# Performance work log

Hardware: AMD Instinct MI355X
Metric: run time of the kernel (lower is better)

Reference implementation:

```python
import jax, jax.numpy as jnp
import numpy as np

H = 2048        # hidden_dim
D = 128         # head_dim
NQ = H // D     # 16 query heads
NKV = 4         # kv heads (GQA)
ROTARY_BASE = 10000.0


def _rope_cos_sin(seq_len, dim, dtype):
    inv_freq = 1.0 / (ROTARY_BASE ** (jnp.arange(0, dim, 2, dtype=jnp.float32) / dim))
    t = jnp.arange(seq_len, dtype=jnp.float32)
    freqs = jnp.outer(t, inv_freq)          # [S, D/2]
    return jnp.cos(freqs).astype(dtype), jnp.sin(freqs).astype(dtype)


def _apply_rope(x, cos, sin):
    # x: [B, S, H, D], non-interleaved (rotate-half) convention of flash-attn
    d2 = x.shape[-1] // 2
    x1, x2 = x[..., :d2], x[..., d2:]
    c = cos[None, :, None, :]
    s = sin[None, :, None, :]
    return jnp.concatenate([x1 * c - x2 * s, x2 * c + x1 * s], axis=-1)


def setup_inputs() -> dict:
    key = jax.random.key(0)
    ks = jax.random.split(key, 9)
    B, S = 2, 2048
    sd = 1.0 / np.sqrt(H)
    return {
        "hidden_states": jax.random.normal(ks[0], (B, S, H), jnp.float32),
        "Wq": jax.random.normal(ks[1], (H, NQ * D), jnp.float32) * sd,
        "bq": jnp.zeros((NQ * D,), jnp.float32),
        "Wk": jax.random.normal(ks[2], (H, NKV * D), jnp.float32) * sd,
        "bk": jnp.zeros((NKV * D,), jnp.float32),
        "Wv": jax.random.normal(ks[3], (H, NKV * D), jnp.float32) * sd,
        "bv": jnp.zeros((NKV * D,), jnp.float32),
        "Wc": jax.random.normal(ks[4], (NQ * D, H), jnp.float32) * sd,
        "bc": jnp.zeros((H,), jnp.float32),
    }


def reference(hidden_states, Wq, bq, Wk, bk, Wv, bv, Wc, bc):
    B, S, _ = hidden_states.shape
    scale = 1.0 / np.sqrt(D)  # scale_attn_by_inverse_layer_idx=False

    q = (hidden_states @ Wq + bq).reshape(B, S, NQ, D)
    k = (hidden_states @ Wk + bk).reshape(B, S, NKV, D)
    v = (hidden_states @ Wv + bv).reshape(B, S, NKV, D)

    cos, sin = _rope_cos_sin(S, D, q.dtype)
    q = _apply_rope(q, cos, sin)
    k = _apply_rope(k, cos, sin)

    # GQA: expand kv heads to match query heads
    rep = NQ // NKV
    k_e = jnp.repeat(k, rep, axis=2)  # [B, S, NQ, D]
    v_e = jnp.repeat(v, rep, axis=2)

    scores = jnp.einsum("bshd,bthd->bhst", q, k_e) * scale  # [B, NQ, S, S]
    causal = jnp.tril(jnp.ones((S, S), bool))
    scores = jnp.where(causal[None, None], scores, jnp.finfo(scores.dtype).min)
    probs = jax.nn.softmax(scores, axis=-1)
    attn = jnp.einsum("bhst,bthd->bshd", probs, v_e)  # [B, S, NQ, D]

    out = attn.reshape(B, S, NQ * D) @ Wc + bc  # resid dropout p=0 (eval)
    return out, k, v
```

## Files before the change

### kernel.cpp

```cpp
#include <hip/hip_runtime.h>
#include <math.h>

typedef unsigned short u16;
typedef __attribute__((ext_vector_type(8))) short s16x8;
typedef __attribute__((ext_vector_type(4))) float f32x4;
typedef __attribute__((ext_vector_type(16))) float f32x16;

#define B_  2
#define S_  2048
#define H_  2048
#define D_  128
#define NQ_ 16
#define NKV_ 4
#define M_  (B_*S_)
#define NQKV_ 3072

#define MFMA16(a,b,c) __builtin_amdgcn_mfma_f32_16x16x32_bf16(a,b,c,0,0,0)
#define MFMA32(a,b,c) __builtin_amdgcn_mfma_f32_32x32x16_bf16(a,b,c,0,0,0)

__device__ __forceinline__ u16 f2bf(float x) {
  union { float f; unsigned u; } v; v.f = x;
  unsigned r = v.u + 0x7fffu + ((v.u >> 16) & 1u);
  return (u16)(r >> 16);
}
__device__ __forceinline__ float bf2f(u16 x) {
  union { unsigned u; float f; } v; v.u = ((unsigned)x) << 16;
  return v.f;
}

__device__ __forceinline__ unsigned cvtpk(float lo, float hi) {
  unsigned r;
  asm("v_cvt_pk_bf16_f32 %0, %1, %2" : "=v"(r) : "v"(lo), "v"(hi));
  return r;
}

__global__ __launch_bounds__(256) void cvt_x(const float* __restrict__ X, u16* __restrict__ Xb, long n4) {
  const f32x4* X4 = (const f32x4*)X;
  for (long i = (long)blockIdx.x*256 + threadIdx.x; i < n4; i += (long)gridDim.x*256) {
    f32x4 v = X4[i];
    union { u16 u[4]; unsigned long long ll; } p;
    p.u[0] = f2bf(v[0]); p.u[1] = f2bf(v[1]); p.u[2] = f2bf(v[2]); p.u[3] = f2bf(v[3]);
    ((unsigned long long*)Xb)[i] = p.ll;
  }
}

__global__ __launch_bounds__(256) void wtrans(const float* __restrict__ W, u16* __restrict__ Wt,
                                              int N, int K) {
  __shared__ float t[32][33];
  const int n0 = blockIdx.x*32, k0 = blockIdx.y*32;
  const int tx = threadIdx.x, ty = threadIdx.y;
  #pragma unroll
  for (int i = 0; i < 32; i += 8) t[ty+i][tx] = W[(long)(k0+ty+i)*N + n0 + tx];
  __syncthreads();
  #pragma unroll
  for (int i = 0; i < 32; i += 8) Wt[(long)(n0+ty+i)*K + k0 + tx] = f2bf(t[tx][ty+i]);
}

__global__ __launch_bounds__(256) void vtrans(const u16* __restrict__ QKV, u16* __restrict__ Vt) {
  __shared__ u16 t[32][33];
  const int bk = blockIdx.z;
  const int s0 = blockIdx.x*32, d0 = blockIdx.y*32;
  const int tx = threadIdx.x, ty = threadIdx.y;
  const int b = bk >> 2, kvh = bk & 3;
  #pragma unroll
  for (int i = 0; i < 32; i += 8)
    t[ty+i][tx] = QKV[(long)(b*S_ + s0+ty+i)*NQKV_ + 2560 + kvh*128 + d0 + tx];
  __syncthreads();
  #pragma unroll
  for (int i = 0; i < 32; i += 8)
    Vt[((long)bk*D_ + d0+ty+i)*S_ + s0 + tx] = t[tx][ty+i];
}

__global__ void concat_bias(const float* bq, const float* bk, const float* bv, float* bqkv) {
  int i = blockIdx.x*256 + threadIdx.x;
  if (i < NQKV_)
    bqkv[i] = (i < 2048) ? bq[i] : ((i < 2560) ? bk[i-2048] : bv[i-2560]);
}

__global__ void rope_tab(float* __restrict__ cosb, float* __restrict__ sinb) {
  int i = blockIdx.x*256 + threadIdx.x;
  int t = i >> 6, d = i & 63;
  float inv = powf(10000.0f, -((float)(2*d)) * (1.0f/128.0f));
  float fr = (float)t * inv;
  float sv, cv;
  sincosf(fr, &sv, &cv);
  cosb[i] = cv; sinb[i] = sv;
}

__global__ __launch_bounds__(256) void rope_qkv(
    const u16* __restrict__ QKV, const float* __restrict__ cosb, const float* __restrict__ sinb,
    u16* __restrict__ Qb, u16* __restrict__ Kb,
    float* __restrict__ kout, float* __restrict__ vout)
{
  const float QS = 0.08838834764831845f * 1.4426950408889634f;
  const int m = blockIdx.x;
  const int b = m >> 11, s = m & 2047;
  const int tid = threadIdx.x;
  const u16* row = QKV + (long)m * NQKV_;
  const int d = tid & 63;
  const float c  = cosb[s*64 + d];
  const float sn = sinb[s*64 + d];
  #pragma unroll
  for (int i = 0; i < 4; i++) {
    int hh = (tid + i*256) >> 6;
    float x1 = bf2f(row[hh*128 + d]), x2 = bf2f(row[hh*128 + d + 64]);
    float o1 = x1*c - x2*sn, o2 = x2*c + x1*sn;
    long base = ((long)(b*NQ_ + hh)*S_ + s)*D_;
    Qb[base + d] = f2bf(o1*QS);
    Qb[base + d + 64] = f2bf(o2*QS);
  }
  {
    int kh = tid >> 6;
    float x1 = bf2f(row[2048 + kh*128 + d]), x2 = bf2f(row[2048 + kh*128 + d + 64]);
    float o1 = x1*c - x2*sn, o2 = x2*c + x1*sn;
    long kb = ((long)(b*NKV_ + kh)*S_ + s)*D_;
    Kb[kb + d] = f2bf(o1);
    Kb[kb + d + 64] = f2bf(o2);
    long ko = ((long)m*NKV_ + kh)*D_;
    kout[ko + d] = o1;
    kout[ko + d + 64] = o2;
  }
  #pragma unroll
  for (int i = 0; i < 2; i++) {
    int e = tid + i*256;
    vout[(long)m*512 + e] = bf2f(row[2560 + e]);
  }
}

template<int BN, typename OutT>
__global__ __launch_bounds__(512, 2) void gemm256(
    const u16* __restrict__ A, const u16* __restrict__ Bm,
    const float* __restrict__ bias, OutT* __restrict__ C,
    int M, int N, int K)
{
  __shared__ u16 As[2][256*64];
  __shared__ u16 Bs[2][BN*64];
  constexpr int WCc = (BN == 256) ? 4 : 2;
  constexpr int MI  = (BN == 256) ? 8 : 4;
  constexpr int LB  = BN/64;
  constexpr int TOT = 4 + LB;

  const int tid = threadIdx.x;
  const int lane = tid & 63, w = tid >> 6;
  const int r16 = lane & 15, g = lane >> 4;
  const int wrn = w / WCc, wcn = w % WCc;
  const int abase = wrn * (MI*16);
  const int bbase = wcn * 64;

  const int gx = gridDim.x;
  const int nwg = gx * gridDim.y;
  const int id = blockIdx.y * gx + blockIdx.x;
  const int cpx = nwg >> 3;
  const int sid = (id & 7) * cpx + (id >> 3);
  const long m0 = (long)(sid / gx) * 256;
  const long n0 = (long)(sid % gx) * BN;

  const u16* Ag = A + m0 * K;
  const u16* Bg = Bm + n0 * K;

  auto stage = [&](int buf, int k0) {
    #pragma unroll
    for (int i = 0; i < 4; i++) {
      const int slot = i*512 + tid;
      const int row = slot >> 3, cg = slot & 7;
      const u16* src = Ag + (long)row*K + k0 + ((cg ^ (row & 7)) * 8);
      __builtin_amdgcn_global_load_lds(
          (const __attribute__((address_space(1))) unsigned int*)src,
          (__attribute__((address_space(3))) unsigned int*)&As[buf][slot*8], 16, 0, 0);
    }
    #pragma unroll
    for (int i = 0; i < LB; i++) {
      const int slot = i*512 + tid;
      const int row = slot >> 3, cg = slot & 7;
      const u16* src = Bg + (long)row*K + k0 + ((cg ^ (row & 7)) * 8);
      __builtin_amdgcn_global_load_lds(
          (const __attribute__((address_space(1))) unsigned int*)src,
          (__attribute__((address_space(3))) unsigned int*)&Bs[buf][slot*8], 16, 0, 0);
    }
  };

  f32x4 acc[MI][4] = {};
  const int nt = K >> 6;

  stage(0, 0);
  stage(1, 64);
  for (int t = 0; t < nt; t++) {
    if (t + 1 < nt) {
      if constexpr (TOT == 8) asm volatile("s_waitcnt vmcnt(8)" ::: "memory");
      else                    asm volatile("s_waitcnt vmcnt(6)" ::: "memory");
    } else {
      asm volatile("s_waitcnt vmcnt(0)" ::: "memory");
    }
    __builtin_amdgcn_s_barrier();

    const u16* as = &As[t & 1][0];
    const u16* bs = &Bs[t & 1][0];
    #pragma unroll
    for (int k = 0; k < 2; k++) {
      s16x8 bfr[4];
      #pragma unroll
      for (int nj = 0; nj < 4; nj++) {
        const int R = bbase + nj*16 + r16;
        bfr[nj] = *(const s16x8*)&bs[R*64 + (((k*4 + g) ^ (R & 7)) * 8)];
      }
      __builtin_amdgcn_s_setprio(1);
      #pragma unroll
      for (int mi = 0; mi < MI; mi++) {
        const int R = abase + mi*16 + r16;
        s16x8 afr = *(const s16x8*)&as[R*64 + (((k*4 + g) ^ (R & 7)) * 8)];
        #pragma unroll
        for (int nj = 0; nj < 4; nj++)
          acc[mi][nj] = MFMA16(afr, bfr[nj], acc[mi][nj]);
      }
      __builtin_amdgcn_s_setprio(0);
    }
    __builtin_amdgcn_s_barrier();
    if (t + 2 < nt) stage(t & 1, (t + 2) << 6);
  }

  #pragma unroll
  for (int mi = 0; mi < MI; mi++) {
    #pragma unroll
    for (int nj = 0; nj < 4; nj++) {
      const int col = bbase + nj*16 + r16;
      const float bv = bias[n0 + col];
      #pragma unroll
      for (int r = 0; r < 4; r++) {
        const long row = m0 + abase + mi*16 + g*4 + r;
        if constexpr (sizeof(OutT) == 2)
          C[row * N + n0 + col] = (OutT)f2bf(acc[mi][nj][r] + bv);
        else
          C[row * N + n0 + col] = (OutT)(acc[mi][nj][r] + bv);
      }
    }
  }
}

__global__ __launch_bounds__(256, 2) void attn_kernel(
    const u16* __restrict__ Qb, const u16* __restrict__ Kb,
    const u16* __restrict__ Vt, u16* __restrict__ Ob)
{
  __shared__ u16 Ks[2][64*128];
  __shared__ u16 Vs[2][128*64];
  const int tid = threadIdx.x;
  const int lane = tid & 63, w = tid >> 6;
  const int l31 = lane & 31, hi = lane >> 5;
  const int id = blockIdx.x;
  const int bh = id & 31;
  const int b = bh >> 4, h = bh & 15;
  const int p = id >> 5;
  const int qt = (p < 8) ? p : (23 - p);
  const int kvh = h >> 2;
  const int q0w = qt*128 + w*32;
  const int nt = 2*qt + 2;

  const u16* Qg = Qb + (((long)(b*NQ_ + h))*S_ + q0w)*D_;
  const u16* Kg = Kb + ((long)(b*NKV_ + kvh))*S_*D_;
  const u16* Vg = Vt + ((long)(b*NKV_ + kvh))*D_*S_;

  s16x8 qf[8];
  #pragma unroll
  for (int ks = 0; ks < 8; ks++)
    qf[ks] = *(const s16x8*)&Qg[l31*D_ + ks*16 + hi*8];

  f32x16 po[4] = {};
  float mrow = -1e30f, lrow = 0.f;

  auto stage = [&](int buf, int kv0s) {
    #pragma unroll
    for (int i = 0; i < 4; i++) {
      const int c = i*4 + w;
      const int G = c*64 + lane;
      const int krow = G >> 4, kcg = G & 15;
      const u16* gk = Kg + (long)(kv0s + krow)*D_ + ((kcg ^ (krow & 15)) * 8);
      __builtin_amdgcn_global_load_lds(
          (const __attribute__((address_space(1))) unsigned int*)gk,
          (__attribute__((address_space(3))) unsigned int*)&Ks[buf][c*512], 16, 0, 0);
      const int vrow = G >> 3, vcg = G & 7;
      const u16* gv = Vg + (long)vrow*S_ + kv0s + ((vcg ^ (vrow & 7)) * 8);
      __builtin_amdgcn_global_load_lds(
          (const __attribute__((address_space(1))) unsigned int*)gv,
          (__attribute__((address_space(3))) unsigned int*)&Vs[buf][c*512], 16, 0, 0);
    }
  };

  stage(0, 0);
  for (int t = 0; t < nt; t++) {
    const int cur = t & 1;
    const int kv0 = t*64;
    if (t + 1 < nt) {
      stage(cur ^ 1, kv0 + 64);
      asm volatile("s_waitcnt vmcnt(8)" ::: "memory");
    } else {
      asm volatile("s_waitcnt vmcnt(0)" ::: "memory");
    }
    __builtin_amdgcn_s_barrier();

    if (kv0 <= q0w + 31) {
      f32x16 sc[2] = {};
      #pragma unroll
      for (int ks = 0; ks < 8; ks++) {
        #pragma unroll
        for (int ct = 0; ct < 2; ct++) {
          const int row = ct*32 + l31;
          s16x8 kf = *(const s16x8*)&Ks[cur][row*128 + ((ks*16 + hi*8) ^ ((row & 15)*8))];
          sc[ct] = MFMA32(kf, qf[ks], sc[ct]);
        }
      }
      if (kv0 + 63 > q0w) {
        const int qrow = q0w + l31;
        #pragma unroll
        for (int ct = 0; ct < 2; ct++)
          #pragma unroll
          for (int r = 0; r < 16; r++) {
            int kv = kv0 + ct*32 + (r & 3) + 8*(r >> 2) + 4*hi;
            if (kv > qrow) sc[ct][r] = -3.0e38f;
          }
      }
      float pm = sc[0][0];
      #pragma unroll
      for (int ct = 0; ct < 2; ct++)
        #pragma unroll
        for (int r = 0; r < 16; r++) pm = fmaxf(pm, sc[ct][r]);
      pm = fmaxf(pm, __shfl_xor(pm, 32, 64));
      if (!__all(pm - mrow <= 8.0f)) {
        float mn = fmaxf(mrow, pm);
        float fr = exp2f(mrow - mn);
        mrow = mn;
        lrow *= fr;
        #pragma unroll
        for (int r = 0; r < 16; r++) {
          float frv = __shfl(fr, (r & 3) + 8*(r >> 2) + 4*hi, 64);
          #pragma unroll
          for (int dt = 0; dt < 4; dt++) po[dt][r] *= frv;
        }
      }
      float ps = 0.f;
      #pragma unroll
      for (int ct = 0; ct < 2; ct++)
        #pragma unroll
        for (int r = 0; r < 16; r++) {
          float pv = exp2f(sc[ct][r] - mrow);
          sc[ct][r] = pv;
          ps += pv;
        }
      ps += __shfl_xor(ps, 32, 64);
      lrow += ps;
      unsigned mw[2][8], ex[2][8];
      #pragma unroll
      for (int ct = 0; ct < 2; ct++)
        #pragma unroll
        for (int wd = 0; wd < 8; wd++)
          mw[ct][wd] = cvtpk(sc[ct][2*wd], sc[ct][2*wd + 1]);
      #pragma unroll
      for (int ct = 0; ct < 2; ct++)
        #pragma unroll
        for (int wd = 0; wd < 8; wd++)
          ex[ct][wd] = __shfl_xor((int)mw[ct][wd], 32, 64);
      s16x8 pa[4];
      #pragma unroll
      for (int ct = 0; ct < 2; ct++)
        #pragma unroll
        for (int pp = 0; pp < 2; pp++) {
          union { unsigned u[4]; s16x8 v; } pu;
          pu.u[0] = hi ? ex[ct][4*pp + 2] : mw[ct][4*pp + 0];
          pu.u[1] = hi ? ex[ct][4*pp + 3] : mw[ct][4*pp + 1];
          pu.u[2] = hi ? mw[ct][4*pp + 2] : ex[ct][4*pp + 0];
          pu.u[3] = hi ? mw[ct][4*pp + 3] : ex[ct][4*pp + 1];
          pa[ct*2 + pp] = pu.v;
        }
      #pragma unroll
      for (int ks2 = 0; ks2 < 4; ks2++)
        #pragma unroll
        for (int dt = 0; dt < 4; dt++) {
          const int row = dt*32 + l31;
          s16x8 vf = *(const s16x8*)&Vs[cur][row*64 + ((ks2*16 + hi*8) ^ ((row & 7)*8))];
          po[dt] = MFMA32(pa[ks2], vf, po[dt]);
        }
    }
    __builtin_amdgcn_s_barrier();
  }

  float inv = 1.0f / lrow;
  #pragma unroll
  for (int r = 0; r < 16; r++) {
    const int qr = (r & 3) + 8*(r >> 2) + 4*hi;
    float invq = __shfl(inv, qr, 64);
    const long q = (long)q0w + qr;
    #pragma unroll
    for (int dt = 0; dt < 4; dt++)
      Ob[((long)b*S_ + q)*H_ + h*D_ + dt*32 + l31] = f2bf(po[dt][r]*invq);
  }
}

extern "C" void kernel_launch(void* const* d_in, const int* in_sizes, int n_in,
                              void* d_out, int out_size, void* d_ws, size_t ws_size,
                              hipStream_t stream) {
  const float* hs = (const float*)d_in[0];
  const float* Wq = (const float*)d_in[1];
  const float* bq = (const float*)d_in[2];
  const float* Wk = (const float*)d_in[3];
  const float* bk = (const float*)d_in[4];
  const float* Wv = (const float*)d_in[5];
  const float* bv = (const float*)d_in[6];
  const float* Wc = (const float*)d_in[7];
  const float* bc = (const float*)d_in[8];

  float* out  = (float*)d_out;
  float* kout = out + (long)M_*H_;
  float* vout = kout + (long)M_*NKV_*D_;

  char* ws = (char*)d_ws;
  u16*  Xbf   = (u16*)ws;
  u16*  Wqkvt = Xbf + (long)M_*H_;
  u16*  Wct   = Wqkvt + (long)NQKV_*H_;
  float* bqkv = (float*)(Wct + (long)H_*H_);
  u16*  QKV   = (u16*)(bqkv + NQKV_);
  float* cosb = (float*)(QKV + (long)M_*NQKV_);
  float* sinb = cosb + S_*64;
  u16*  Qbf   = (u16*)(sinb + S_*64);
  u16*  Kbf   = Qbf + (long)B_*NQ_*S_*D_;
  u16*  Vtb   = Kbf + (long)B_*NKV_*S_*D_;
  u16*  Obf   = Vtb + (long)B_*NKV_*D_*S_;

  cvt_x<<<2048, 256, 0, stream>>>(hs, Xbf, (long)M_*H_/4);
  wtrans<<<dim3(64,64), dim3(32,8), 0, stream>>>(Wq, Wqkvt, 2048, 2048);
  wtrans<<<dim3(16,64), dim3(32,8), 0, stream>>>(Wk, Wqkvt + 2048L*2048, 512, 2048);
  wtrans<<<dim3(16,64), dim3(32,8), 0, stream>>>(Wv, Wqkvt + 2560L*2048, 512, 2048);
  wtrans<<<dim3(64,64), dim3(32,8), 0, stream>>>(Wc, Wct, 2048, 2048);
  concat_bias<<<12, 256, 0, stream>>>(bq, bk, bv, bqkv);
  rope_tab<<<512, 256, 0, stream>>>(cosb, sinb);

  gemm256<256, u16><<<dim3(NQKV_/256, M_/256), 512, 0, stream>>>(
      Xbf, Wqkvt, bqkv, QKV, M_, NQKV_, H_);
  rope_qkv<<<M_, 256, 0, stream>>>(QKV, cosb, sinb, Qbf, Kbf, kout, vout);
  vtrans<<<dim3(S_/32, D_/32, B_*NKV_), dim3(32,8), 0, stream>>>(QKV, Vtb);
  attn_kernel<<<dim3(512), 256, 0, stream>>>(Qbf, Kbf, Vtb, Obf);
  gemm256<128, float><<<dim3(H_/128, M_/256), 512, 0, stream>>>(
      Obf, Wct, bc, out, M_, H_, H_);
}
```

Measured before the change: 229.3 us.

## Split long causal attention tiles across two blocks and merge partials

Query tiles 8-15, which have the longest causal KV ranges, are now split into two halves processed by separate blocks. Each half writes unnormalized fp32 partial outputs plus running max and sum, and a new merge kernel combines them. The grid grows from 512 to 768 blocks to improve load balance. The change also relayouts V in shared memory with a new swizzle and replaces the shuffle-based P fragment exchange with permlane32_swap. In exchange it adds an extra kernel launch and fp32 partial-output traffic to global memory.

Measured after the change: 242.2 us. 1.06x slower.

```diff
diff --git a/kernel.cpp b/kernel.cpp
--- a/kernel.cpp
+++ b/kernel.cpp
@@ -5,6 +5,7 @@
 typedef __attribute__((ext_vector_type(8))) short s16x8;
 typedef __attribute__((ext_vector_type(4))) float f32x4;
 typedef __attribute__((ext_vector_type(16))) float f32x16;
+typedef unsigned u32x2u __attribute__((ext_vector_type(2)));
 
 #define B_  2
 #define S_  2048
@@ -32,6 +33,20 @@
   unsigned r;
   asm("v_cvt_pk_bf16_f32 %0, %1, %2" : "=v"(r) : "v"(lo), "v"(hi));
   return r;
+}
+
+__device__ __forceinline__ void plswap(unsigned &x, unsigned &y) {
+#if __has_builtin(__builtin_amdgcn_permlane32_swap)
+  u32x2u r = __builtin_amdgcn_permlane32_swap(x, y, false, false);
+  x = r[0]; y = r[1];
+#else
+  const bool hb = (threadIdx.x & 32) != 0;
+  unsigned ex = (unsigned)__shfl_xor((int)x, 32, 64);
+  unsigned ey = (unsigned)__shfl_xor((int)y, 32, 64);
+  unsigned nx = hb ? ey : x;
+  unsigned ny = hb ? y : ex;
+  x = nx; y = ny;
+#endif
 }
 
 __global__ __launch_bounds__(256) void cvt_x(const float* __restrict__ X, u16* __restrict__ Xb, long n4) {
@@ -238,21 +253,32 @@
 
 __global__ __launch_bounds__(256, 2) void attn_kernel(
     const u16* __restrict__ Qb, const u16* __restrict__ Kb,
-    const u16* __restrict__ Vt, u16* __restrict__ Ob)
+    const u16* __restrict__ Vt, u16* __restrict__ Ob,
+    float* __restrict__ Opart, float* __restrict__ Ml)
 {
   __shared__ u16 Ks[2][64*128];
-  __shared__ u16 Vs[2][128*64];
+  __shared__ u16 Vs[2][64*128];
   const int tid = threadIdx.x;
   const int lane = tid & 63, w = tid >> 6;
   const int l31 = lane & 31, hi = lane >> 5;
   const int id = blockIdx.x;
   const int bh = id & 31;
   const int b = bh >> 4, h = bh & 15;
-  const int p = id >> 5;
-  const int qt = (p < 8) ? p : (23 - p);
+  const int jj = id >> 5;
+  int qt, t0, t1, part;
+  if (jj < 16) {
+    qt = 8 + (jj >> 1);
+    const int half = jj & 1;
+    t0 = half ? (qt + 1) : 0;
+    t1 = half ? (2*qt + 2) : (qt + 1);
+    part = (bh*8 + (qt - 8))*2 + half;
+  } else {
+    qt = jj - 16;
+    t0 = 0; t1 = 2*qt + 2;
+    part = -1;
+  }
   const int kvh = h >> 2;
   const int q0w = qt*128 + w*32;
-  const int nt = 2*qt + 2;
 
   const u16* Qg = Qb + (((long)(b*NQ_ + h))*S_ + q0w)*D_;
   const u16* Kg = Kb + ((long)(b*NKV_ + kvh))*S_*D_;
@@ -276,20 +302,23 @@
       __builtin_amdgcn_global_load_lds(
           (const __attribute__((address_space(1))) unsigned int*)gk,
           (__attribute__((address_space(3))) unsigned int*)&Ks[buf][c*512], 16, 0, 0);
-      const int vrow = G >> 3, vcg = G & 7;
-      const u16* gv = Vg + (long)vrow*S_ + kv0s + ((vcg ^ (vrow & 7)) * 8);
+      const int o = c*512 + lane*8;
+      const int d2 = o >> 7, t16 = (o >> 3) & 15;
+      const int gidx = t16 ^ (d2 & 15);
+      const int dsr = ((gidx >> 3) << 6) + d2;
+      const u16* gv = Vg + (long)dsr*S_ + kv0s + ((gidx & 7) * 8);
       __builtin_amdgcn_global_load_lds(
           (const __attribute__((address_space(1))) unsigned int*)gv,
           (__attribute__((address_space(3))) unsigned int*)&Vs[buf][c*512], 16, 0, 0);
     }
   };
 
-  stage(0, 0);
-  for (int t = 0; t < nt; t++) {
-    const int cur = t & 1;
+  stage(0, t0*64);
+  for (int t = t0; t < t1; t++) {
+    const int cur = (t - t0) & 1;
     const int kv0 = t*64;
-    if (t + 1 < nt) {
-      stage(cur ^ 1, kv0 + 64);
+    if (t + 1 < t1) {
+      stage(cur ^ 1, (t + 1)*64);
       asm volatile("s_waitcnt vmcnt(8)" ::: "memory");
     } else {
       asm volatile("s_waitcnt vmcnt(0)" ::: "memory");
@@ -346,50 +375,94 @@
         }
       ps += __shfl_xor(ps, 32, 64);
       lrow += ps;
-      unsigned mw[2][8], ex[2][8];
+      unsigned mw[2][8];
       #pragma unroll
       for (int ct = 0; ct < 2; ct++)
         #pragma unroll
         for (int wd = 0; wd < 8; wd++)
           mw[ct][wd] = cvtpk(sc[ct][2*wd], sc[ct][2*wd + 1]);
+      s16x8 pa[4];
       #pragma unroll
       for (int ct = 0; ct < 2; ct++)
         #pragma unroll
-        for (int wd = 0; wd < 8; wd++)
-          ex[ct][wd] = __shfl_xor((int)mw[ct][wd], 32, 64);
-      s16x8 pa[4];
-      #pragma unroll
-      for (int ct = 0; ct < 2; ct++)
-        #pragma unroll
         for (int pp = 0; pp < 2; pp++) {
+          unsigned a0 = mw[ct][4*pp + 0], b0 = mw[ct][4*pp + 2];
+          unsigned a1 = mw[ct][4*pp + 1], b1 = mw[ct][4*pp + 3];
+          plswap(a0, b0);
+          plswap(a1, b1);
           union { unsigned u[4]; s16x8 v; } pu;
-          pu.u[0] = hi ? ex[ct][4*pp + 2] : mw[ct][4*pp + 0];
-          pu.u[1] = hi ? ex[ct][4*pp + 3] : mw[ct][4*pp + 1];
-          pu.u[2] = hi ? mw[ct][4*pp + 2] : ex[ct][4*pp + 0];
-          pu.u[3] = hi ? mw[ct][4*pp + 3] : ex[ct][4*pp + 1];
+          pu.u[0] = a0; pu.u[1] = a1; pu.u[2] = b0; pu.u[3] = b1;
           pa[ct*2 + pp] = pu.v;
         }
       #pragma unroll
       for (int ks2 = 0; ks2 < 4; ks2++)
         #pragma unroll
         for (int dt = 0; dt < 4; dt++) {
-          const int row = dt*32 + l31;
-          s16x8 vf = *(const s16x8*)&Vs[cur][row*64 + ((ks2*16 + hi*8) ^ ((row & 7)*8))];
+          const int d = dt*32 + l31, d2 = d & 63;
+          const int gidx = ((d >> 6) << 3) + ks2*2 + hi;
+          s16x8 vf = *(const s16x8*)&Vs[cur][d2*128 + ((gidx ^ (d2 & 15)) * 8)];
           po[dt] = MFMA32(pa[ks2], vf, po[dt]);
         }
     }
     __builtin_amdgcn_s_barrier();
   }
 
-  float inv = 1.0f / lrow;
-  #pragma unroll
-  for (int r = 0; r < 16; r++) {
-    const int qr = (r & 3) + 8*(r >> 2) + 4*hi;
-    float invq = __shfl(inv, qr, 64);
-    const long q = (long)q0w + qr;
-    #pragma unroll
-    for (int dt = 0; dt < 4; dt++)
-      Ob[((long)b*S_ + q)*H_ + h*D_ + dt*32 + l31] = f2bf(po[dt][r]*invq);
+  if (part >= 0) {
+    float* Od = Opart + (long)part * (128*128);
+    #pragma unroll
+    for (int r = 0; r < 16; r++) {
+      const int qr = w*32 + (r & 3) + 8*(r >> 2) + 4*hi;
+      #pragma unroll
+      for (int dt = 0; dt < 4; dt++)
+        Od[qr*128 + dt*32 + l31] = po[dt][r];
+    }
+    if (hi == 0) {
+      Ml[((long)part*128 + w*32 + l31)*2 + 0] = mrow;
+      Ml[((long)part*128 + w*32 + l31)*2 + 1] = lrow;
+    }
+  } else {
+    float inv = 1.0f / lrow;
+    #pragma unroll
+    for (int r = 0; r < 16; r++) {
+      const int qr = (r & 3) + 8*(r >> 2) + 4*hi;
+      float invq = __shfl(inv, qr, 64);
+      const long q = (long)q0w + qr;
+      #pragma unroll
+      for (int dt = 0; dt < 4; dt++)
+        Ob[((long)b*S_ + q)*H_ + h*D_ + dt*32 + l31] = f2bf(po[dt][r]*invq);
+    }
+  }
+}
+
+__global__ __launch_bounds__(256) void attn_merge(
+    const float* __restrict__ Opart, const float* __restrict__ Ml, u16* __restrict__ Ob)
+{
+  const int tile = blockIdx.x;
+  const int bh = tile >> 3;
+  const int qt = 8 + (tile & 7);
+  const int b = bh >> 4, h = bh & 15;
+  const int t = threadIdx.x;
+  const int row = t >> 1, ch = t & 1;
+  const long p0 = (long)(tile*2) * (128*128);
+  const long p1 = p0 + 128*128;
+  const float m0 = Ml[((long)(tile*2)*128 + row)*2 + 0];
+  const float l0 = Ml[((long)(tile*2)*128 + row)*2 + 1];
+  const float m1 = Ml[((long)(tile*2+1)*128 + row)*2 + 0];
+  const float l1 = Ml[((long)(tile*2+1)*128 + row)*2 + 1];
+  const float m = fmaxf(m0, m1);
+  const float f0 = exp2f(m0 - m), f1 = exp2f(m1 - m);
+  const float inv = 1.0f / (l0*f0 + l1*f1);
+  const float* O0 = Opart + p0 + row*128 + ch*64;
+  const float* O1 = Opart + p1 + row*128 + ch*64;
+  u16* dst = Ob + ((long)b*S_ + qt*128 + row)*H_ + h*D_ + ch*64;
+  #pragma unroll
+  for (int c = 0; c < 64; c += 4) {
+    f32x4 a = *(const f32x4*)&O0[c];
+    f32x4 bb = *(const f32x4*)&O1[c];
+    union { u16 u[4]; unsigned long long ll; } pk;
+    #pragma unroll
+    for (int j = 0; j < 4; j++) pk.u[j] = f2bf((a[j]*f0 + bb[j]*f1) * inv);
+    *(unsigned long long*)&dst[c] = pk.ll;
   }
 }
 
@@ -422,6 +495,8 @@
   u16*  Kbf   = Qbf + (long)B_*NQ_*S_*D_;
   u16*  Vtb   = Kbf + (long)B_*NKV_*S_*D_;
   u16*  Obf   = Vtb + (long)B_*NKV_*D_*S_;
+  float* Opart = (float*)(Obf + (long)M_*H_);
+  float* Mlb   = Opart + (long)512*128*128;
 
   cvt_x<<<2048, 256, 0, stream>>>(hs, Xbf, (long)M_*H_/4);
   wtrans<<<dim3(64,64), dim3(32,8), 0, stream>>>(Wq, Wqkvt, 2048, 2048);
@@ -435,7 +510,8 @@
       Xbf, Wqkvt, bqkv, QKV, M_, NQKV_, H_);
   rope_qkv<<<M_, 256, 0, stream>>>(QKV, cosb, sinb, Qbf, Kbf, kout, vout);
   vtrans<<<dim3(S_/32, D_/32, B_*NKV_), dim3(32,8), 0, stream>>>(QKV, Vtb);
-  attn_kernel<<<dim3(512), 256, 0, stream>>>(Qbf, Kbf, Vtb, Obf);
+  attn_kernel<<<dim3(768), 256, 0, stream>>>(Qbf, Kbf, Vtb, Obf, Opart, Mlb);
+  attn_merge<<<dim3(256), 256, 0, stream>>>(Opart, Mlb, Obf);
   gemm256<128, float><<<dim3(H_/128, M_/256), 512, 0, stream>>>(
       Obf, Wct, bc, out, M_, H_, H_);
 }
```

## Restructure attention loop with static double buffers, permlane swap, setprio, new V swizzle

Applied to the files above, without the earlier changes.

Unrolls the attention KV loop by two so buffer indices are compile-time constants and moves the per-tile work into a compute lambda. The P-matrix half exchange now uses permlane32_swap instead of 16 shuffles plus selects. MFMA sections are wrapped in s_setprio, the V LDS tile gets a new 128-wide swizzled layout, and the tile schedule now issues the heaviest causal q-tiles first. The aim is to cut address arithmetic, cross-lane traffic and LDS bank conflicts and to improve load balance, at the cost of more complex indexing that must stay correct for the V layout.

New measurement: 221.8 us. 3.3% less time.

```diff
diff --git a/kernel.cpp b/kernel.cpp
--- a/kernel.cpp
+++ b/kernel.cpp
@@ -5,6 +5,7 @@
 typedef __attribute__((ext_vector_type(8))) short s16x8;
 typedef __attribute__((ext_vector_type(4))) float f32x4;
 typedef __attribute__((ext_vector_type(16))) float f32x16;
+typedef unsigned u32x2u __attribute__((ext_vector_type(2)));
 
 #define B_  2
 #define S_  2048
@@ -32,6 +33,20 @@
   unsigned r;
   asm("v_cvt_pk_bf16_f32 %0, %1, %2" : "=v"(r) : "v"(lo), "v"(hi));
   return r;
+}
+
+__device__ __forceinline__ void plswap(unsigned &x, unsigned &y) {
+#if __has_builtin(__builtin_amdgcn_permlane32_swap)
+  u32x2u r = __builtin_amdgcn_permlane32_swap(x, y, false, false);
+  x = r[0]; y = r[1];
+#else
+  const bool hb = (threadIdx.x & 32) != 0;
+  unsigned ex = (unsigned)__shfl_xor((int)x, 32, 64);
+  unsigned ey = (unsigned)__shfl_xor((int)y, 32, 64);
+  unsigned nx = hb ? ey : x;
+  unsigned ny = hb ? y : ex;
+  x = nx; y = ny;
+#endif
 }
 
 __global__ __launch_bounds__(256) void cvt_x(const float* __restrict__ X, u16* __restrict__ Xb, long n4) {
@@ -241,7 +256,7 @@
     const u16* __restrict__ Vt, u16* __restrict__ Ob)
 {
   __shared__ u16 Ks[2][64*128];
-  __shared__ u16 Vs[2][128*64];
+  __shared__ u16 Vs[2][64*128];
   const int tid = threadIdx.x;
   const int lane = tid & 63, w = tid >> 6;
   const int l31 = lane & 31, hi = lane >> 5;
@@ -249,7 +264,7 @@
   const int bh = id & 31;
   const int b = bh >> 4, h = bh & 15;
   const int p = id >> 5;
-  const int qt = (p < 8) ? p : (23 - p);
+  const int qt = (p < 8) ? (15 - p) : (p - 8);
   const int kvh = h >> 2;
   const int q0w = qt*128 + w*32;
   const int nt = 2*qt + 2;
@@ -276,108 +291,118 @@
       __builtin_amdgcn_global_load_lds(
           (const __attribute__((address_space(1))) unsigned int*)gk,
           (__attribute__((address_space(3))) unsigned int*)&Ks[buf][c*512], 16, 0, 0);
-      const int vrow = G >> 3, vcg = G & 7;
-      const u16* gv = Vg + (long)vrow*S_ + kv0s + ((vcg ^ (vrow & 7)) * 8);
+      const int o = c*512 + lane*8;
+      const int d2 = o >> 7, t16 = (o >> 3) & 15;
+      const int gidx = t16 ^ (d2 & 15);
+      const int dsr = ((gidx >> 3) << 6) + d2;
+      const u16* gv = Vg + (long)dsr*S_ + kv0s + ((gidx & 7) * 8);
       __builtin_amdgcn_global_load_lds(
           (const __attribute__((address_space(1))) unsigned int*)gv,
           (__attribute__((address_space(3))) unsigned int*)&Vs[buf][c*512], 16, 0, 0);
     }
   };
 
+  auto compute = [&](int buf, int t) {
+    const int kv0 = t*64;
+    if (kv0 > q0w + 31) return;
+    f32x16 sc[2] = {};
+    __builtin_amdgcn_s_setprio(1);
+    #pragma unroll
+    for (int ks = 0; ks < 8; ks++) {
+      #pragma unroll
+      for (int ct = 0; ct < 2; ct++) {
+        const int row = ct*32 + l31;
+        s16x8 kf = *(const s16x8*)&Ks[buf][row*128 + ((ks*16 + hi*8) ^ ((row & 15)*8))];
+        sc[ct] = MFMA32(kf, qf[ks], sc[ct]);
+      }
+    }
+    __builtin_amdgcn_s_setprio(0);
+    if (kv0 + 63 > q0w) {
+      const int qrow = q0w + l31;
+      #pragma unroll
+      for (int ct = 0; ct < 2; ct++)
+        #pragma unroll
+        for (int r = 0; r < 16; r++) {
+          int kv = kv0 + ct*32 + (r & 3) + 8*(r >> 2) + 4*hi;
+          if (kv > qrow) sc[ct][r] = -3.0e38f;
+        }
+    }
+    float pm = sc[0][0];
+    #pragma unroll
+    for (int ct = 0; ct < 2; ct++)
+      #pragma unroll
+      for (int r = 0; r < 16; r++) pm = fmaxf(pm, sc[ct][r]);
+    pm = fmaxf(pm, __shfl_xor(pm, 32, 64));
+    if (!__all(pm - mrow <= 8.0f)) {
+      float mn = fmaxf(mrow, pm);
+      float fr = exp2f(mrow - mn);
+      mrow = mn;
+      lrow *= fr;
+      #pragma unroll
+      for (int r = 0; r < 16; r++) {
+        float frv = __shfl(fr, (r & 3) + 8*(r >> 2) + 4*hi, 64);
+        #pragma unroll
+        for (int dt = 0; dt < 4; dt++) po[dt][r] *= frv;
+      }
+    }
+    float ps = 0.f;
+    #pragma unroll
+    for (int ct = 0; ct < 2; ct++)
+      #pragma unroll
+      for (int r = 0; r < 16; r++) {
+        float pv = exp2f(sc[ct][r] - mrow);
+        sc[ct][r] = pv;
+        ps += pv;
+      }
+    ps += __shfl_xor(ps, 32, 64);
+    lrow += ps;
+    unsigned mw[2][8];
+    #pragma unroll
+    for (int ct = 0; ct < 2; ct++)
+      #pragma unroll
+      for (int wd = 0; wd < 8; wd++)
+        mw[ct][wd] = cvtpk(sc[ct][2*wd], sc[ct][2*wd + 1]);
+    s16x8 pa[4];
+    #pragma unroll
+    for (int ct = 0; ct < 2; ct++)
+      #pragma unroll
+      for (int pp = 0; pp < 2; pp++) {
+        unsigned a0 = mw[ct][4*pp + 0], b0 = mw[ct][4*pp + 2];
+        unsigned a1 = mw[ct][4*pp + 1], b1 = mw[ct][4*pp + 3];
+        plswap(a0, b0);
+        plswap(a1, b1);
+        union { unsigned u[4]; s16x8 v; } pu;
+        pu.u[0] = a0; pu.u[1] = a1; pu.u[2] = b0; pu.u[3] = b1;
+        pa[ct*2 + pp] = pu.v;
+      }
+    __builtin_amdgcn_s_setprio(1);
+    #pragma unroll
+    for (int ks2 = 0; ks2 < 4; ks2++)
+      #pragma unroll
+      for (int dt = 0; dt < 4; dt++) {
+        const int d = dt*32 + l31, d2 = d & 63;
+        const int gidx = ((d >> 6) << 3) + ks2*2 + hi;
+        s16x8 vf = *(const s16x8*)&Vs[buf][d2*128 + ((gidx ^ (d2 & 15)) * 8)];
+        po[dt] = MFMA32(pa[ks2], vf, po[dt]);
+      }
+    __builtin_amdgcn_s_setprio(0);
+  };
+
   stage(0, 0);
-  for (int t = 0; t < nt; t++) {
-    const int cur = t & 1;
-    const int kv0 = t*64;
-    if (t + 1 < nt) {
-      stage(cur ^ 1, kv0 + 64);
+  for (int t = 0; t < nt; t += 2) {
+    stage(1, (t + 1)*64);
+    asm volatile("s_waitcnt vmcnt(8)" ::: "memory");
+    __builtin_amdgcn_s_barrier();
+    compute(0, t);
+    __builtin_amdgcn_s_barrier();
+    if (t + 2 < nt) {
+      stage(0, (t + 2)*64);
       asm volatile("s_waitcnt vmcnt(8)" ::: "memory");
     } else {
       asm volatile("s_waitcnt vmcnt(0)" ::: "memory");
     }
     __builtin_amdgcn_s_barrier();
-
-    if (kv0 <= q0w + 31) {
-      f32x16 sc[2] = {};
-      #pragma unroll
-      for (int ks = 0; ks < 8; ks++) {
-        #pragma unroll
-        for (int ct = 0; ct < 2; ct++) {
-          const int row = ct*32 + l31;
-          s16x8 kf = *(const s16x8*)&Ks[cur][row*128 + ((ks*16 + hi*8) ^ ((row & 15)*8))];
-          sc[ct] = MFMA32(kf, qf[ks], sc[ct]);
-        }
-      }
-      if (kv0 + 63 > q0w) {
-        const int qrow = q0w + l31;
-        #pragma unroll
-        for (int ct = 0; ct < 2; ct++)
-          #pragma unroll
-          for (int r = 0; r < 16; r++) {
-            int kv = kv0 + ct*32 + (r & 3) + 8*(r >> 2) + 4*hi;
-            if (kv > qrow) sc[ct][r] = -3.0e38f;
-          }
-      }
-      float pm = sc[0][0];
-      #pragma unroll
-      for (int ct = 0; ct < 2; ct++)
-        #pragma unroll
-        for (int r = 0; r < 16; r++) pm = fmaxf(pm, sc[ct][r]);
-      pm = fmaxf(pm, __shfl_xor(pm, 32, 64));
-      if (!__all(pm - mrow <= 8.0f)) {
-        float mn = fmaxf(mrow, pm);
-        float fr = exp2f(mrow - mn);
-        mrow = mn;
-        lrow *= fr;
-        #pragma unroll
-        for (int r = 0; r < 16; r++) {
-          float frv = __shfl(fr, (r & 3) + 8*(r >> 2) + 4*hi, 64);
-          #pragma unroll
-          for (int dt = 0; dt < 4; dt++) po[dt][r] *= frv;
-        }
-      }
-      float ps = 0.f;
-      #pragma unroll
-      for (int ct = 0; ct < 2; ct++)
-        #pragma unroll
-        for (int r = 0; r < 16; r++) {
-          float pv = exp2f(sc[ct][r] - mrow);
-          sc[ct][r] = pv;
-          ps += pv;
-        }
-      ps += __shfl_xor(ps, 32, 64);
-      lrow += ps;
-      unsigned mw[2][8], ex[2][8];
-      #pragma unroll
-      for (int ct = 0; ct < 2; ct++)
-        #pragma unroll
-        for (int wd = 0; wd < 8; wd++)
-          mw[ct][wd] = cvtpk(sc[ct][2*wd], sc[ct][2*wd + 1]);
-      #pragma unroll
-      for (int ct = 0; ct < 2; ct++)
-        #pragma unroll
-        for (int wd = 0; wd < 8; wd++)
-          ex[ct][wd] = __shfl_xor((int)mw[ct][wd], 32, 64);
-      s16x8 pa[4];
-      #pragma unroll
-      for (int ct = 0; ct < 2; ct++)
-        #pragma unroll
-        for (int pp = 0; pp < 2; pp++) {
-          union { unsigned u[4]; s16x8 v; } pu;
-          pu.u[0] = hi ? ex[ct][4*pp + 2] : mw[ct][4*pp + 0];
-          pu.u[1] = hi ? ex[ct][4*pp + 3] : mw[ct][4*pp + 1];
-          pu.u[2] = hi ? mw[ct][4*pp + 2] : ex[ct][4*pp + 0];
-          pu.u[3] = hi ? mw[ct][4*pp + 3] : ex[ct][4*pp + 1];
-          pa[ct*2 + pp] = pu.v;
-        }
-      #pragma unroll
-      for (int ks2 = 0; ks2 < 4; ks2++)
-        #pragma unroll
-        for (int dt = 0; dt < 4; dt++) {
-          const int row = dt*32 + l31;
-          s16x8 vf = *(const s16x8*)&Vs[cur][row*64 + ((ks2*16 + hi*8) ^ ((row & 7)*8))];
-          po[dt] = MFMA32(pa[ks2], vf, po[dt]);
-        }
-    }
+    compute(1, t + 1);
     __builtin_amdgcn_s_barrier();
   }
 
```
